# Optimization experiments

Measured on AMD Instinct MI355X. Metric: run time of the kernel, lower is better.

The kernel has to match this reference:

```python
import jax, jax.numpy as jnp
import numpy as np

B, N, K, C = 16, 1024, 64, 128
TEMPERATURE = 0.07


def _l2_normalize(x, eps=1e-12):
    # matches torch F.normalize(dim=-1): x / max(||x||, eps)
    n = jnp.linalg.norm(x, axis=-1, keepdims=True)
    return x / jnp.maximum(n, eps)


def setup_inputs() -> dict:
    key = jax.random.key(0)
    k1, k2, k3, k4 = jax.random.split(key, 4)
    q = jax.random.normal(k1, (B, N, C), dtype=jnp.float32)
    k = jax.random.normal(k2, (B, N, C), dtype=jnp.float32)
    positive_indices = jax.random.randint(k3, (B, N), 0, N)
    negative_indices = jax.random.randint(k4, (B, N, K), 0, N)
    return {"q": q, "k": k,
            "positive_indices": positive_indices,
            "negative_indices": negative_indices}


def reference(q, k, positive_indices, negative_indices):
    qn = _l2_normalize(q)                                   # (B,N,C)
    kn = _l2_normalize(k)                                   # (B,N,C)

    pos_valid = positive_indices >= 0                       # (B,N)
    pos_idx = jnp.where(pos_valid, positive_indices, 0)
    positive = jnp.take_along_axis(kn, pos_idx[..., None], axis=1)  # (B,N,C)
    pos_sim = jnp.sum(qn * positive, axis=-1) / TEMPERATURE          # (B,N)

    neg_valid = negative_indices >= 0                       # (B,N,K)
    neg_idx = jnp.where(neg_valid, negative_indices, 0)
    # batched ragged gather of negatives: (B,N,K,C)
    negs = jax.vmap(lambda kb, idx: kb[idx])(kn, neg_idx)
    neg_sim = jnp.einsum('bnc,bnkc->bnk', qn, negs) / TEMPERATURE    # (B,N,K)
    neg_sim = jnp.where(neg_valid, neg_sim, -jnp.inf)

    # cross-entropy with label 0 over [pos, negs]:
    # loss = logsumexp(logits) - pos_sim
    logits = jnp.concatenate([pos_sim[..., None], neg_sim], axis=-1)  # (B,N,1+K)
    per_patch = jax.nn.logsumexp(logits, axis=-1) - pos_sim           # (B,N)

    total = jnp.sum(jnp.where(pos_valid, per_patch, 0.0))
    count = jnp.sum(pos_valid)
    return jnp.where(count > 0, total / jnp.maximum(count, 1), 0.0)
```

## Files before the change

kernel.cpp:

```cpp
#include <hip/hip_runtime.h>
#include <math.h>

#define B_ 16
#define N_ 1024
#define K_ 64
#define C_ 128
#define INV_T 14.285714285714286f
#define NBLK_MAIN 2048

using f32x2 = __attribute__((ext_vector_type(2))) float;

__device__ __forceinline__ float waveReduceSum(float v) {
#pragma unroll
    for (int off = 32; off > 0; off >>= 1)
        v += __shfl_xor(v, off, 64);
    return v;
}

__device__ __forceinline__ unsigned short f2bf(float x) {
    unsigned u = __float_as_uint(x);
    return (unsigned short)((u + 0x7fffu + ((u >> 16) & 1u)) >> 16);
}
__device__ __forceinline__ float bflo(unsigned u) { return __uint_as_float(u << 16); }
__device__ __forceinline__ float bfhi(unsigned u) { return __uint_as_float(u & 0xffff0000u); }

__global__ __launch_bounds__(256) void normalize_kernel(
    const float* __restrict__ q, const float* __restrict__ k,
    unsigned short* __restrict__ qn, unsigned char* __restrict__ kn) {
    const int lane = threadIdx.x & 63;
    const int wid  = threadIdx.x >> 6;
    const int base = blockIdx.x * 16 + wid * 4;
#pragma unroll
    for (int r = 0; r < 4; ++r) {
        const int row = base + r;
        const bool is_q = row < (B_ * N_);
        const int  rr   = is_q ? row : row - B_ * N_;
        const float* src = (is_q ? q : k) + (size_t)rr * C_;
        const float2 v = *(const float2*)(src + 2 * lane);
        const float ss = waveReduceSum(v.x * v.x + v.y * v.y);
        const float inv = 1.0f / fmaxf(sqrtf(ss), 1e-12f);
        if (is_q) {
            const float sc = inv * INV_T;
            ushort2 o; o.x = f2bf(v.x * sc); o.y = f2bf(v.y * sc);
            *(ushort2*)(qn + (size_t)rr * C_ + 2 * lane) = o;
        } else {
            const int pk = __builtin_amdgcn_cvt_pk_fp8_f32(v.x * inv, v.y * inv, 0, false);
            *(unsigned short*)(kn + (size_t)rr * C_ + 2 * lane) =
                (unsigned short)(pk & 0xffff);
        }
    }
}

__global__ __launch_bounds__(256, 4) void infonce_kernel(
    const unsigned short* __restrict__ qn, const unsigned char* __restrict__ kn,
    const int* __restrict__ pos_idx, const int* __restrict__ neg_idx,
    float* __restrict__ partials) {
    __shared__ float wave_tot[4], wave_cnt[4];

    const int lane = threadIdx.x & 63;
    const int wid  = threadIdx.x >> 6;
    const int g    = lane >> 3;
    const int s    = lane & 7;

    const int batch = blockIdx.x & 15;
    const int chunk = blockIdx.x >> 4;
    const int rbase = chunk * 8 + wid * 2;

    const unsigned char* kb = kn + (size_t)batch * (N_ * C_);

    float tot = 0.0f, cnt = 0.0f;

#pragma unroll
    for (int r = 0; r < 2; ++r) {
        const int n   = rbase + r;
        const int row = batch * N_ + n;

        const unsigned short* qrow = qn + (size_t)row * C_;
        f32x2 qf[8];
#pragma unroll
        for (int i = 0; i < 2; ++i) {
            const uint4 qu = *(const uint4*)(qrow + s * 16 + i * 8);
            qf[i*4+0] = f32x2{bflo(qu.x), bfhi(qu.x)};
            qf[i*4+1] = f32x2{bflo(qu.y), bfhi(qu.y)};
            qf[i*4+2] = f32x2{bflo(qu.z), bfhi(qu.z)};
            qf[i*4+3] = f32x2{bflo(qu.w), bfhi(qu.w)};
        }

        const int  pidx = pos_idx[row];
        const bool pval = pidx >= 0;
        const int  p0   = pval ? pidx : 0;

        const int* nrow = neg_idx + (size_t)row * K_;
        int nidx[8];
#pragma unroll
        for (int p = 0; p < 8; ++p) nidx[p] = nrow[p * 8 + g];

        float d[9];
#pragma unroll
        for (int p = 0; p < 9; ++p) {
            const unsigned char* kr =
                (p < 8) ? kb + (size_t)(nidx[p] >= 0 ? nidx[p] : 0) * C_
                        : kb + (size_t)p0 * C_;
            const uint4 ku = *(const uint4*)(kr + s * 16);
            const unsigned w[4] = {ku.x, ku.y, ku.z, ku.w};
            f32x2 acc = f32x2{0.0f, 0.0f};
#pragma unroll
            for (int i = 0; i < 4; ++i) {
                const f32x2 lo = __builtin_amdgcn_cvt_pk_f32_fp8(w[i], false);
                const f32x2 hi = __builtin_amdgcn_cvt_pk_f32_fp8(w[i], true);
                acc = lo * qf[i*2+0] + acc;
                acc = hi * qf[i*2+1] + acc;
            }
            float dot = acc[0] + acc[1];
            dot += __shfl_xor(dot, 1, 64);
            dot += __shfl_xor(dot, 2, 64);
            dot += __shfl_xor(dot, 4, 64);
            d[p] = dot;
        }

        const float pos_sim = d[8];

        float simv[8];
#pragma unroll
        for (int p = 0; p < 8; ++p)
            simv[p] = (nidx[p] >= 0) ? d[p] : -INFINITY;

        float m = pos_sim;
#pragma unroll
        for (int p = 0; p < 8; ++p) m = fmaxf(m, simv[p]);
        m = fmaxf(m, __shfl_xor(m, 8, 64));
        m = fmaxf(m, __shfl_xor(m, 16, 64));
        m = fmaxf(m, __shfl_xor(m, 32, 64));

        float ssum = 0.0f;
#pragma unroll
        for (int p = 0; p < 8; ++p) ssum += __expf(simv[p] - m);
        ssum += __shfl_xor(ssum, 8, 64);
        ssum += __shfl_xor(ssum, 16, 64);
        ssum += __shfl_xor(ssum, 32, 64);
        ssum += __expf(pos_sim - m);

        const float per_patch = m + __logf(ssum) - pos_sim;
        if (pval) { tot += per_patch; cnt += 1.0f; }
    }

    if (lane == 0) { wave_tot[wid] = tot; wave_cnt[wid] = cnt; }
    __syncthreads();
    if (threadIdx.x == 0) {
        partials[2 * blockIdx.x]     = wave_tot[0] + wave_tot[1] + wave_tot[2] + wave_tot[3];
        partials[2 * blockIdx.x + 1] = wave_cnt[0] + wave_cnt[1] + wave_cnt[2] + wave_cnt[3];
    }
}

__global__ __launch_bounds__(256) void finalize_kernel(const float* __restrict__ partials,
                                                       float* __restrict__ out, int nblocks) {
    __shared__ float st[256], sc[256];
    float t = 0.0f, c = 0.0f;
    for (int i = threadIdx.x; i < nblocks; i += 256) {
        t += partials[2 * i];
        c += partials[2 * i + 1];
    }
    st[threadIdx.x] = t;
    sc[threadIdx.x] = c;
    __syncthreads();
    for (int off = 128; off > 0; off >>= 1) {
        if (threadIdx.x < off) {
            st[threadIdx.x] += st[threadIdx.x + off];
            sc[threadIdx.x] += sc[threadIdx.x + off];
        }
        __syncthreads();
    }
    if (threadIdx.x == 0) {
        const float cntv = sc[0];
        out[0] = (cntv > 0.0f) ? st[0] / fmaxf(cntv, 1.0f) : 0.0f;
    }
}

extern "C" void kernel_launch(void* const* d_in, const int* in_sizes, int n_in,
                              void* d_out, int out_size, void* d_ws, size_t ws_size,
                              hipStream_t stream) {
    const float* q   = (const float*)d_in[0];
    const float* k   = (const float*)d_in[1];
    const int*   pos = (const int*)d_in[2];
    const int*   neg = (const int*)d_in[3];
    float* out = (float*)d_out;

    float* wsf = (float*)d_ws;
    float* partials = wsf;
    unsigned short* qn = (unsigned short*)(wsf + 8192);
    unsigned char*  kn = (unsigned char*)(qn + (size_t)B_ * N_ * C_);

    normalize_kernel<<<2048, 256, 0, stream>>>(q, k, qn, kn);
    infonce_kernel<<<NBLK_MAIN, 256, 0, stream>>>(qn, kn, pos, neg, partials);
    finalize_kernel<<<1, 256, 0, stream>>>(partials, out, NBLK_MAIN);
}
```

Baseline: 86.16 us.

## Fuse q normalization into main kernel and finalize via last-block ticket

Drops the bf16 q-normalization pass: the main kernel now reads raw fp32 q rows, computes their norm with an 8-lane shuffle reduction and scales them in registers. The normalize kernel shrinks to handle only k, which it writes as fp8 and also uses to reset a ticket counter. The separate finalize launch is replaced by an atomic ticket, so the last block to finish reduces all partials. This removes one launch and the qn write/read round trip, but each q row is now read as fp32 (double the bytes of bf16), and the main kernel gains shared memory for the final reduction.

```diff
diff --git a/kernel.cpp b/kernel.cpp
--- a/kernel.cpp
+++ b/kernel.cpp
@@ -17,45 +17,33 @@
     return v;
 }
 
-__device__ __forceinline__ unsigned short f2bf(float x) {
-    unsigned u = __float_as_uint(x);
-    return (unsigned short)((u + 0x7fffu + ((u >> 16) & 1u)) >> 16);
-}
-__device__ __forceinline__ float bflo(unsigned u) { return __uint_as_float(u << 16); }
-__device__ __forceinline__ float bfhi(unsigned u) { return __uint_as_float(u & 0xffff0000u); }
-
-__global__ __launch_bounds__(256) void normalize_kernel(
-    const float* __restrict__ q, const float* __restrict__ k,
-    unsigned short* __restrict__ qn, unsigned char* __restrict__ kn) {
+__global__ __launch_bounds__(256) void knorm_kernel(
+    const float* __restrict__ k, unsigned char* __restrict__ kn,
+    unsigned* __restrict__ ticket) {
+    if (blockIdx.x == 0 && threadIdx.x == 0) *ticket = 0u;
     const int lane = threadIdx.x & 63;
     const int wid  = threadIdx.x >> 6;
     const int base = blockIdx.x * 16 + wid * 4;
 #pragma unroll
     for (int r = 0; r < 4; ++r) {
         const int row = base + r;
-        const bool is_q = row < (B_ * N_);
-        const int  rr   = is_q ? row : row - B_ * N_;
-        const float* src = (is_q ? q : k) + (size_t)rr * C_;
-        const float2 v = *(const float2*)(src + 2 * lane);
+        const float2 v = *(const float2*)(k + (size_t)row * C_ + 2 * lane);
         const float ss = waveReduceSum(v.x * v.x + v.y * v.y);
         const float inv = 1.0f / fmaxf(sqrtf(ss), 1e-12f);
-        if (is_q) {
-            const float sc = inv * INV_T;
-            ushort2 o; o.x = f2bf(v.x * sc); o.y = f2bf(v.y * sc);
-            *(ushort2*)(qn + (size_t)rr * C_ + 2 * lane) = o;
-        } else {
-            const int pk = __builtin_amdgcn_cvt_pk_fp8_f32(v.x * inv, v.y * inv, 0, false);
-            *(unsigned short*)(kn + (size_t)rr * C_ + 2 * lane) =
-                (unsigned short)(pk & 0xffff);
-        }
+        const int pk = __builtin_amdgcn_cvt_pk_fp8_f32(v.x * inv, v.y * inv, 0, false);
+        *(unsigned short*)(kn + (size_t)row * C_ + 2 * lane) =
+            (unsigned short)(pk & 0xffff);
     }
 }
 
 __global__ __launch_bounds__(256, 4) void infonce_kernel(
-    const unsigned short* __restrict__ qn, const unsigned char* __restrict__ kn,
+    const float* __restrict__ q, const unsigned char* __restrict__ kn,
     const int* __restrict__ pos_idx, const int* __restrict__ neg_idx,
-    float* __restrict__ partials) {
+    float* __restrict__ partials, unsigned* __restrict__ ticket,
+    float* __restrict__ out) {
     __shared__ float wave_tot[4], wave_cnt[4];
+    __shared__ float st[256], sc2[256];
+    __shared__ unsigned is_last;
 
     const int lane = threadIdx.x & 63;
     const int wid  = threadIdx.x >> 6;
@@ -75,16 +63,25 @@
         const int n   = rbase + r;
         const int row = batch * N_ + n;
 
-        const unsigned short* qrow = qn + (size_t)row * C_;
+        const float* qrow = q + (size_t)row * C_;
         f32x2 qf[8];
+        f32x2 qacc = f32x2{0.0f, 0.0f};
 #pragma unroll
-        for (int i = 0; i < 2; ++i) {
-            const uint4 qu = *(const uint4*)(qrow + s * 16 + i * 8);
-            qf[i*4+0] = f32x2{bflo(qu.x), bfhi(qu.x)};
-            qf[i*4+1] = f32x2{bflo(qu.y), bfhi(qu.y)};
-            qf[i*4+2] = f32x2{bflo(qu.z), bfhi(qu.z)};
-            qf[i*4+3] = f32x2{bflo(qu.w), bfhi(qu.w)};
+        for (int i = 0; i < 4; ++i) {
+            const float4 v = *(const float4*)(qrow + s * 16 + i * 4);
+            qf[i*2+0] = f32x2{v.x, v.y};
+            qf[i*2+1] = f32x2{v.z, v.w};
+            qacc = qf[i*2+0] * qf[i*2+0] + qacc;
+            qacc = qf[i*2+1] * qf[i*2+1] + qacc;
         }
+        float qss = qacc[0] + qacc[1];
+        qss += __shfl_xor(qss, 1, 64);
+        qss += __shfl_xor(qss, 2, 64);
+        qss += __shfl_xor(qss, 4, 64);
+        const float sc = (1.0f / fmaxf(sqrtf(qss), 1e-12f)) * INV_T;
+        const f32x2 scv = f32x2{sc, sc};
+#pragma unroll
+        for (int i = 0; i < 8; ++i) qf[i] *= scv;
 
         const int  pidx = pos_idx[row];
         const bool pval = pidx >= 0;
@@ -149,30 +146,33 @@
     if (threadIdx.x == 0) {
         partials[2 * blockIdx.x]     = wave_tot[0] + wave_tot[1] + wave_tot[2] + wave_tot[3];
         partials[2 * blockIdx.x + 1] = wave_cnt[0] + wave_cnt[1] + wave_cnt[2] + wave_cnt[3];
+        __threadfence();
+        const unsigned old = atomicAdd(ticket, 1u);
+        is_last = (old == NBLK_MAIN - 1) ? 1u : 0u;
     }
-}
+    __syncthreads();
 
-__global__ __launch_bounds__(256) void finalize_kernel(const float* __restrict__ partials,
-                                                       float* __restrict__ out, int nblocks) {
-    __shared__ float st[256], sc[256];
-    float t = 0.0f, c = 0.0f;
-    for (int i = threadIdx.x; i < nblocks; i += 256) {
-        t += partials[2 * i];
-        c += partials[2 * i + 1];
-    }
-    st[threadIdx.x] = t;
-    sc[threadIdx.x] = c;
-    __syncthreads();
-    for (int off = 128; off > 0; off >>= 1) {
-        if (threadIdx.x < off) {
-            st[threadIdx.x] += st[threadIdx.x + off];
-            sc[threadIdx.x] += sc[threadIdx.x + off];
+    if (is_last) {
+        __threadfence();
+        float t = 0.0f, c = 0.0f;
+        for (int i = threadIdx.x; i < NBLK_MAIN; i += 256) {
+            t += partials[2 * i];
+            c += partials[2 * i + 1];
         }
+        st[threadIdx.x]  = t;
+        sc2[threadIdx.x] = c;
         __syncthreads();
-    }
-    if (threadIdx.x == 0) {
-        const float cntv = sc[0];
-        out[0] = (cntv > 0.0f) ? st[0] / fmaxf(cntv, 1.0f) : 0.0f;
+        for (int off = 128; off > 0; off >>= 1) {
+            if (threadIdx.x < off) {
+                st[threadIdx.x]  += st[threadIdx.x + off];
+                sc2[threadIdx.x] += sc2[threadIdx.x + off];
+            }
+            __syncthreads();
+        }
+        if (threadIdx.x == 0) {
+            const float cntv = sc2[0];
+            out[0] = (cntv > 0.0f) ? st[0] / fmaxf(cntv, 1.0f) : 0.0f;
+        }
     }
 }
 
@@ -186,11 +186,11 @@
     float* out = (float*)d_out;
 
     float* wsf = (float*)d_ws;
-    float* partials = wsf;
-    unsigned short* qn = (unsigned short*)(wsf + 8192);
-    unsigned char*  kn = (unsigned char*)(qn + (size_t)B_ * N_ * C_);
+    float*    partials = wsf;
+    unsigned* ticket   = (unsigned*)(wsf + 4096);
+    unsigned char* kn  = (unsigned char*)(wsf + 8192);
 
-    normalize_kernel<<<2048, 256, 0, stream>>>(q, k, qn, kn);
-    infonce_kernel<<<NBLK_MAIN, 256, 0, stream>>>(qn, kn, pos, neg, partials);
-    finalize_kernel<<<1, 256, 0, stream>>>(partials, out, NBLK_MAIN);
+    knorm_kernel<<<1024, 256, 0, stream>>>(k, kn, ticket);
+    infonce_kernel<<<NBLK_MAIN, 256, 0, stream>>>(q, kn, pos, neg,
+                                                  partials, ticket, out);
 }
```

Result: slower. 124.3 us (+44.3%).
